# Performance work log

Hardware: AMD Instinct MI355X
Metric: run time of the kernel (lower is better)

The kernel has to match this reference:

```python
import jax, jax.numpy as jnp
import numpy as np

HIDDEN = 100
LAYERS = 10
B, T = 512, 512
INIT = 0.1  # 1/sqrt(hidden_size), torch default uniform bound


def setup_inputs() -> dict:
    key = jax.random.key(0)
    ks = jax.random.split(key, 9)
    u = lambda k, shape: jax.random.uniform(k, shape, jnp.float32, -INIT, INIT)
    return {
        "x": jax.random.normal(ks[0], (B, T, 1), jnp.float32),
        "hidden_state": jnp.zeros((LAYERS, B, HIDDEN), jnp.float32),
        "W_ih0": u(ks[1], (HIDDEN, 1)),
        "W_ih": u(ks[2], (LAYERS - 1, HIDDEN, HIDDEN)),
        "W_hh": u(ks[3], (LAYERS, HIDDEN, HIDDEN)),
        "b_ih": u(ks[4], (LAYERS, HIDDEN)),
        "b_hh": u(ks[5], (LAYERS, HIDDEN)),
        "W_out": u(ks[6], (1, HIDDEN)),
        "b_out": u(ks[7], (1,)),
    }


def reference(x, hidden_state, W_ih0, W_ih, W_hh, b_ih, b_hh, W_out, b_out):
    # Multi-layer tanh RNN (batch_first). Scan over time; fixed loop over 10 layers.
    def step(h, x_t):  # h: [L, B, H], x_t: [B, 1]
        inp = x_t
        new_h = []
        for l in range(LAYERS):
            Wi = W_ih0 if l == 0 else W_ih[l - 1]
            hl = jnp.tanh(inp @ Wi.T + b_ih[l] + h[l] @ W_hh[l].T + b_hh[l])
            new_h.append(hl)
            inp = hl
        return jnp.stack(new_h), inp  # carry, top-layer output [B, H]

    h_final, top = jax.lax.scan(step, hidden_state, jnp.swapaxes(x, 0, 1))
    rnn_output = jnp.swapaxes(top, 0, 1)  # [B, T, H]
    # Per-timestep Linear == one batched matmul
    outs = rnn_output @ W_out.T + b_out  # [B, T, 1]
    return outs, h_final
```

## Files before the change

### kernel.cpp

```cpp
#include <hip/hip_runtime.h>


#define HH   100
#define HS   132
#define HSS  136
#define NL   10
#define NPAIR 5
#define NIF   4
#define BBS  512
#define TTS  512
#define NB   32
#define BC   16
#define NT   512
#define SLOTS (BC * 128)

typedef __attribute__((ext_vector_type(8))) short short8;
typedef __attribute__((ext_vector_type(4))) float f32x4;
typedef __attribute__((ext_vector_type(4))) unsigned int u32x4;

__global__ void init_ws_kernel(int* wsi) {
  int i = blockIdx.x * blockDim.x + threadIdx.x;
  if (i < 16384) wsi[i] = 0;
}

__device__ __forceinline__ int flag_idx(int iface, int chunk) {
  return (iface * NB + chunk) * 16;
}

__device__ __forceinline__ void lds_barrier() {
  __asm__ __volatile__("s_waitcnt lgkmcnt(0)\n\ts_barrier" ::: "memory");
}
__device__ __forceinline__ void ctl_barrier() {
  __asm__ __volatile__("s_barrier" ::: "memory");
}

__device__ __forceinline__ float fast_tanh(float v) {
  float e = __expf(2.0f * v);
  return 1.0f - 2.0f * __builtin_amdgcn_rcpf(e + 1.0f);
}

__device__ __forceinline__ unsigned short bf_rtn(float x) {
  return (unsigned short)((__float_as_uint(x) + 0x8000u) >> 16);
}

__global__ __launch_bounds__(NT, 1) void rnn_pipe(
    const float* __restrict__ x,
    const float* __restrict__ h0,
    const float* __restrict__ Wih0,
    const float* __restrict__ Wih,
    const float* __restrict__ Whh,
    const float* __restrict__ bih,
    const float* __restrict__ bhh,
    const float* __restrict__ Wout,
    const float* __restrict__ bout,
    float* __restrict__ out,
    unsigned short* __restrict__ ring,
    int*   __restrict__ wsi,
    int Kv, int RDv)
{
  const int pair  = blockIdx.x / NB;
  const int chunk = blockIdx.x % NB;
  const int tid   = threadIdx.x;
  const int grp   = tid >> 8;
  const int wtid  = tid & 255;
  const int layer = pair * 2 + grp;
  const int Km = Kv - 1, RDm = RDv - 1;
  const int NE = BC * HH;

  const int wave = wtid >> 6, lane = wtid & 63;
  const int quad = lane >> 4, lp = lane & 15;
  const bool is_l9 = (grp == 1 && pair == NPAIR - 1);

  __shared__ unsigned short hbufL[2][BC][HSS];
  __shared__ unsigned short hbufU[2][BC][HSS];
  __shared__ unsigned short ibufL[2][BC][HSS];
  __shared__ float biasS[2][HS];
  __shared__ float wi0s[HS];
  __shared__ float wouts[HS];
  __shared__ float xin[2][BC];

  for (int i = tid; i < 2 * BC * HSS; i += NT) {
    (&hbufL[0][0][0])[i] = 0; (&hbufU[0][0][0])[i] = 0; (&ibufL[0][0][0])[i] = 0;
  }
  for (int i = wtid; i < HS; i += 256) {
    float bv = 0.f;
    if (i < HH) bv = bih[layer * HH + i] + bhh[layer * HH + i];
    else if (i == 100 && layer == NL - 1) bv = bout[0];
    biasS[grp][i] = bv;
    if (grp == 0) wi0s[i]  = (i < HH) ? Wih0[i] : 0.f;
    else          wouts[i] = (i < HH) ? Wout[i] : 0.f;
  }
  if (tid < BC) { xin[0][tid] = 0.f; xin[1][tid] = 0.f; }
  __syncthreads();
  for (int idx = wtid; idx < NE; idx += 256) {
    unsigned short v =
        bf_rtn(h0[((size_t)layer * BBS + chunk * BC + idx / HH) * HH + idx % HH]);
    if (grp == 0) hbufL[0][idx / HH][idx % HH] = v;
    else          hbufU[1][idx / HH][idx % HH] = v;
  }
  __syncthreads();

  short8 Bf[8][2][2];
  #pragma unroll
  for (int kc = 0; kc < 8; ++kc) {
    #pragma unroll
    for (int ntl = 0; ntl < 2; ++ntl) {
      const int n = wave * 32 + ntl * 16 + lp;
      float wv[8];
      #pragma unroll
      for (int j = 0; j < 8; ++j) {
        const int k = kc * 32 + quad * 8 + j;
        float w = 0.f;
        if (kc < 4) {
          if (k < HH) {
            if (n < HH) w = Whh[(size_t)layer * HH * HH + n * HH + k];
            else if (n == 100 && layer == NL - 1) w = Wout[k];
          }
        } else {
          const int kk = k - 128;
          if (layer > 0 && kk >= 0 && kk < HH && n < HH)
            w = Wih[(size_t)(layer - 1) * HH * HH + n * HH + kk];
        }
        wv[j] = w;
      }
      __attribute__((ext_vector_type(4))) unsigned int p1, p2;
      #pragma unroll
      for (int j2 = 0; j2 < 4; ++j2) {
        unsigned ua = __float_as_uint(wv[2 * j2]), ub = __float_as_uint(wv[2 * j2 + 1]);
        p1[j2] = (ua >> 16) | (ub & 0xFFFF0000u);
        float ra = wv[2 * j2]     - __uint_as_float(ua & 0xFFFF0000u);
        float rb = wv[2 * j2 + 1] - __uint_as_float(ub & 0xFFFF0000u);
        p2[j2] = (__float_as_uint(ra) >> 16) | (__float_as_uint(rb) & 0xFFFF0000u);
      }
      Bf[kc][ntl][0] = __builtin_bit_cast(short8, p1);
      Bf[kc][ntl][1] = __builtin_bit_cast(short8, p2);
    }
  }

  const bool is_cons = (grp == 0 && pair > 0);
  const bool is_prod = (grp == 1 && pair < NPAIR - 1);
  int* prog_in  = is_cons ? wsi + flag_idx(pair - 1, chunk)        : nullptr;
  int* cons_in  = is_cons ? wsi + 8192 + flag_idx(pair - 1, chunk) : nullptr;
  int* prog_out = is_prod ? wsi + flag_idx(pair, chunk)            : nullptr;
  int* cons_out = is_prod ? wsi + 8192 + flag_idx(pair, chunk)     : nullptr;
  unsigned short* ring_in  = is_cons ? ring + (size_t)((pair - 1) * NB + chunk) * RDv * SLOTS : nullptr;
  unsigned short* ring_out = is_prod ? ring + (size_t)(pair * NB + chunk) * RDv * SLOTS       : nullptr;

  const int jcv[2] = { wave * 32 + lp, wave * 32 + 16 + lp };
  const float br[2]  = { biasS[grp][jcv[0]], biasS[grp][jcv[1]] };
  const float w0r[2] = { wi0s[jcv[0]], wi0s[jcv[1]] };
  const float boutv = bout[0];

  f32x4 hreg[2] = {};
  float px = 0.f;
  const int srow = wtid >> 4, scol = (wtid & 15) * 8;

  for (int s = 0; s <= TTS; ++s) {
    const int par = s & 1, nxt = par ^ 1;
    const bool active = (grp == 0) ? (s < TTS) : (s >= 1);
    const int t = (grp == 0) ? s : s - 1;
    const bool bstart = (s < TTS) && ((s & Km) == 0);
    const bool upub   = (s >= 1) && ((s & Km) == 0);

    if (bstart) {
      if (tid == 0 && is_cons) {
        while (__hip_atomic_load(prog_in, __ATOMIC_RELAXED, __HIP_MEMORY_SCOPE_AGENT) < s + Kv)
          __builtin_amdgcn_s_sleep(1);
        (void)__hip_atomic_load(prog_in, __ATOMIC_ACQUIRE, __HIP_MEMORY_SCOPE_AGENT);
      }
      if (tid == 256 && is_prod && s + Kv > RDv) {
        while (__hip_atomic_load(cons_out, __ATOMIC_RELAXED, __HIP_MEMORY_SCOPE_AGENT) < s + Kv - RDv)
          __builtin_amdgcn_s_sleep(1);
      }
      ctl_barrier();
      if (is_cons) {
        u32x4 g = *(const u32x4*)(ring_in + (size_t)(s & RDm) * SLOTS + wtid * 8);
        *(u32x4*)&ibufL[par][srow][scol] = g;
      }
      if (grp == 0 && pair == 0 && s == 0) {
        if (wtid < BC) xin[0][wtid] = x[(size_t)(chunk * BC + wtid) * TTS];
      }
      lds_barrier();
    }

    if (is_prod && s >= 2 && ((s - 1) & Km) != 0) {
      u32x4 v = *(const u32x4*)&hbufU[par][srow][scol];
      *(u32x4*)(ring_out + (size_t)((s - 2) & RDm) * SLOTS + wtid * 8) = v;
    }

    u32x4 pv = {};
    bool pre = false;
    if (is_cons && s < TTS && ((s & Km) != Km) && s + 1 < TTS) {
      pv = *(const u32x4*)(ring_in + (size_t)((s + 1) & RDm) * SLOTS + wtid * 8);
      pre = true;
    }
    if (grp == 0 && pair == 0 && s + 1 < TTS && wtid < BC)
      px = x[(size_t)(chunk * BC + wtid) * TTS + (s + 1)];

    if (active) {
      const unsigned short (*myH)[HSS] = (grp == 0) ? hbufL[par] : hbufU[par];
      const unsigned short (*myI)[HSS] = (grp == 0) ? ibufL[par] : hbufL[par];
      short8 Ah[4], AiS[4];
      #pragma unroll
      for (int kc = 0; kc < 4; ++kc)
        Ah[kc] = *(const short8*)&myH[lp][kc * 32 + quad * 8];
      const bool has_in = (grp == 1) || (pair > 0);
      if (has_in) {
        #pragma unroll
        for (int kc = 0; kc < 4; ++kc)
          AiS[kc] = *(const short8*)&myI[lp][kc * 32 + quad * 8];
      } else {
        #pragma unroll
        for (int kc = 0; kc < 4; ++kc) AiS[kc] = short8{};
      }

      f32x4 a1[2], a2[2] = {}, c1[2] = {}, c2[2] = {};
      #pragma unroll
      for (int ntl = 0; ntl < 2; ++ntl)
        a1[ntl] = (f32x4){br[ntl], br[ntl], br[ntl], br[ntl]};
      if (has_in) {
        #pragma unroll
        for (int kc = 0; kc < 4; ++kc) {
          #pragma unroll
          for (int ntl = 0; ntl < 2; ++ntl) {
            c2[ntl] = __builtin_amdgcn_mfma_f32_16x16x32_bf16(AiS[kc], Bf[kc + 4][ntl][1], c2[ntl], 0, 0, 0);
            c1[ntl] = __builtin_amdgcn_mfma_f32_16x16x32_bf16(AiS[kc], Bf[kc + 4][ntl][0], c1[ntl], 0, 0, 0);
          }
        }
      }
      #pragma unroll
      for (int kc = 0; kc < 4; ++kc) {
        #pragma unroll
        for (int ntl = 0; ntl < 2; ++ntl) {
          a2[ntl] = __builtin_amdgcn_mfma_f32_16x16x32_bf16(Ah[kc], Bf[kc][ntl][1], a2[ntl], 0, 0, 0);
          a1[ntl] = __builtin_amdgcn_mfma_f32_16x16x32_bf16(Ah[kc], Bf[kc][ntl][0], a1[ntl], 0, 0, 0);
        }
      }

      unsigned short (*myHn)[HSS] = (grp == 0) ? hbufL[nxt] : hbufU[nxt];
      #pragma unroll
      for (int ntl = 0; ntl < 2; ++ntl) {
        f32x4 sum = (a1[ntl] + a2[ntl]) + (c1[ntl] + c2[ntl]);
        #pragma unroll
        for (int r = 0; r < 4; ++r) {
          const int m = quad * 4 + r;
          float v = sum[r];
          if (layer == 0) v += xin[par][m] * w0r[ntl];
          if (is_l9 && jcv[ntl] == 100) {
            if (s >= 2)
              out[(size_t)(chunk * BC + m) * TTS + (s - 2)] = v;
          } else {
            float h = fast_tanh(v);
            hreg[ntl][r] = h;
            if (jcv[ntl] < HH) myHn[m][jcv[ntl]] = bf_rtn(h);
          }
        }
      }

      if (t == TTS - 1) {
        #pragma unroll
        for (int ntl = 0; ntl < 2; ++ntl)
          if (jcv[ntl] < HH)
            #pragma unroll
            for (int r = 0; r < 4; ++r)
              out[(size_t)BBS * TTS +
                  ((size_t)layer * BBS + chunk * BC + quad * 4 + r) * HH + jcv[ntl]] =
                  hreg[ntl][r];
      }
    }

    if (pre) *(u32x4*)&ibufL[nxt][srow][scol] = pv;
    if (grp == 0 && pair == 0 && s + 1 < TTS && wtid < BC) xin[nxt][wtid] = px;

    if (upub) {
      lds_barrier();
      if (is_prod) {
        u32x4 v = *(const u32x4*)&hbufU[nxt][srow][scol];
        *(u32x4*)(ring_out + (size_t)((s - 1) & RDm) * SLOTS + wtid * 8) = v;
      }
      __syncthreads();
      if (tid == 256 && is_prod)
        __hip_atomic_store(prog_out, s, __ATOMIC_RELEASE, __HIP_MEMORY_SCOPE_AGENT);
      if (tid == 0 && is_cons)
        __hip_atomic_store(cons_in, s, __ATOMIC_RELAXED, __HIP_MEMORY_SCOPE_AGENT);
    } else {
      lds_barrier();
    }
  }

  if (is_l9) {
    const int b = wtid >> 4, seg = wtid & 15;
    float sacc = 0.f;
    #pragma unroll
    for (int jj = 0; jj < 7; ++jj) {
      const int j = seg * 7 + jj;
      if (j < HH) {
        float h = __uint_as_float((unsigned)hbufU[1][b][j] << 16);
        sacc += h * wouts[j];
      }
    }
    sacc += __shfl_xor(sacc, 1, 16);
    sacc += __shfl_xor(sacc, 2, 16);
    sacc += __shfl_xor(sacc, 4, 16);
    sacc += __shfl_xor(sacc, 8, 16);
    if ((wtid & 15) == 0)
      out[(size_t)(chunk * BC + b) * TTS + (TTS - 1)] = sacc + boutv;
  }
}

extern "C" void kernel_launch(void* const* d_in, const int* in_sizes, int n_in,
                              void* d_out, int out_size, void* d_ws, size_t ws_size,
                              hipStream_t stream) {
  const float* x    = (const float*)d_in[0];
  const float* h0   = (const float*)d_in[1];
  const float* Wih0 = (const float*)d_in[2];
  const float* Wih  = (const float*)d_in[3];
  const float* Whh  = (const float*)d_in[4];
  const float* bih  = (const float*)d_in[5];
  const float* bhh  = (const float*)d_in[6];
  const float* Wout = (const float*)d_in[7];
  const float* bout = (const float*)d_in[8];
  float* out = (float*)d_out;

  int* wsi = (int*)d_ws;
  unsigned short* ring = (unsigned short*)((char*)d_ws + 65536);

  const size_t slot_bytes = (size_t)SLOTS * 2;
  int RDv = 32;
  while (RDv > 2 && 65536 + (size_t)NIF * NB * RDv * slot_bytes > ws_size)
    RDv >>= 1;
  int Kv = RDv / 4;
  if (Kv < 1) Kv = 1;

  hipLaunchKernelGGL(init_ws_kernel, dim3(64), dim3(256), 0, stream, wsi);
  hipLaunchKernelGGL(rnn_pipe, dim3(NPAIR * NB), dim3(NT), 0, stream,
                     x, h0, Wih0, Wih, Whh, bih, bhh, Wout, bout, out, ring, wsi,
                     Kv, RDv);
}
```

Before: 1.056 ms.

## Drop split-bf16 weight residual MFMAs and prefetch ring blocks one step early

Weights were held as a high/low bf16 pair, which doubled the MFMA count on the recurrent critical path. They are now a single round-to-nearest bf16 value, halving the matrix work per step and the weight registers. The block-boundary handshake now waits one step ahead, and the ring read is always prefetched, which removes a barrier and global load from the step's critical path. The cost is reduced weight precision, which may raise error across 512 timesteps and 10 layers.

```diff
diff --git a/kernel.cpp b/kernel.cpp
--- a/kernel.cpp
+++ b/kernel.cpp
@@ -98,9 +98,8 @@
     if (grp == 0) hbufL[0][idx / HH][idx % HH] = v;
     else          hbufU[1][idx / HH][idx % HH] = v;
   }
-  __syncthreads();
-
-  short8 Bf[8][2][2];
+
+  short8 Bf[8][2];
   #pragma unroll
   for (int kc = 0; kc < 8; ++kc) {
     #pragma unroll
@@ -123,17 +122,11 @@
         }
         wv[j] = w;
       }
-      __attribute__((ext_vector_type(4))) unsigned int p1, p2;
-      #pragma unroll
-      for (int j2 = 0; j2 < 4; ++j2) {
-        unsigned ua = __float_as_uint(wv[2 * j2]), ub = __float_as_uint(wv[2 * j2 + 1]);
-        p1[j2] = (ua >> 16) | (ub & 0xFFFF0000u);
-        float ra = wv[2 * j2]     - __uint_as_float(ua & 0xFFFF0000u);
-        float rb = wv[2 * j2 + 1] - __uint_as_float(ub & 0xFFFF0000u);
-        p2[j2] = (__float_as_uint(ra) >> 16) | (__float_as_uint(rb) & 0xFFFF0000u);
-      }
-      Bf[kc][ntl][0] = __builtin_bit_cast(short8, p1);
-      Bf[kc][ntl][1] = __builtin_bit_cast(short8, p2);
+      __attribute__((ext_vector_type(4))) unsigned int p1;
+      #pragma unroll
+      for (int j2 = 0; j2 < 4; ++j2)
+        p1[j2] = (unsigned)bf_rtn(wv[2 * j2]) | ((unsigned)bf_rtn(wv[2 * j2 + 1]) << 16);
+      Bf[kc][ntl] = __builtin_bit_cast(short8, p1);
     }
   }
 
@@ -155,32 +148,38 @@
   float px = 0.f;
   const int srow = wtid >> 4, scol = (wtid & 15) * 8;
 
+  if (tid == 0 && is_cons) {
+    while (__hip_atomic_load(prog_in, __ATOMIC_RELAXED, __HIP_MEMORY_SCOPE_AGENT) < Kv)
+      __builtin_amdgcn_s_sleep(1);
+    (void)__hip_atomic_load(prog_in, __ATOMIC_ACQUIRE, __HIP_MEMORY_SCOPE_AGENT);
+  }
+  ctl_barrier();
+  if (is_cons) {
+    u32x4 g = *(const u32x4*)(ring_in + wtid * 8);
+    *(u32x4*)&ibufL[0][srow][scol] = g;
+  }
+  if (grp == 0 && pair == 0 && wtid < BC)
+    xin[0][wtid] = x[(size_t)(chunk * BC + wtid) * TTS];
+  __syncthreads();
+
   for (int s = 0; s <= TTS; ++s) {
     const int par = s & 1, nxt = par ^ 1;
     const bool active = (grp == 0) ? (s < TTS) : (s >= 1);
     const int t = (grp == 0) ? s : s - 1;
-    const bool bstart = (s < TTS) && ((s & Km) == 0);
-    const bool upub   = (s >= 1) && ((s & Km) == 0);
-
-    if (bstart) {
+    const bool preb = ((s & Km) == Km) && (s + 1 < TTS);
+    const bool upub = (s >= 1) && ((s & Km) == 0);
+
+    if (preb) {
       if (tid == 0 && is_cons) {
-        while (__hip_atomic_load(prog_in, __ATOMIC_RELAXED, __HIP_MEMORY_SCOPE_AGENT) < s + Kv)
+        while (__hip_atomic_load(prog_in, __ATOMIC_RELAXED, __HIP_MEMORY_SCOPE_AGENT) < s + 1 + Kv)
           __builtin_amdgcn_s_sleep(1);
         (void)__hip_atomic_load(prog_in, __ATOMIC_ACQUIRE, __HIP_MEMORY_SCOPE_AGENT);
       }
-      if (tid == 256 && is_prod && s + Kv > RDv) {
-        while (__hip_atomic_load(cons_out, __ATOMIC_RELAXED, __HIP_MEMORY_SCOPE_AGENT) < s + Kv - RDv)
+      if (tid == 256 && is_prod && s + 1 + Kv > RDv) {
+        while (__hip_atomic_load(cons_out, __ATOMIC_RELAXED, __HIP_MEMORY_SCOPE_AGENT) < s + 1 + Kv - RDv)
           __builtin_amdgcn_s_sleep(1);
       }
       ctl_barrier();
-      if (is_cons) {
-        u32x4 g = *(const u32x4*)(ring_in + (size_t)(s & RDm) * SLOTS + wtid * 8);
-        *(u32x4*)&ibufL[par][srow][scol] = g;
-      }
-      if (grp == 0 && pair == 0 && s == 0) {
-        if (wtid < BC) xin[0][wtid] = x[(size_t)(chunk * BC + wtid) * TTS];
-      }
-      lds_barrier();
     }
 
     if (is_prod && s >= 2 && ((s - 1) & Km) != 0) {
@@ -190,7 +189,7 @@
 
     u32x4 pv = {};
     bool pre = false;
-    if (is_cons && s < TTS && ((s & Km) != Km) && s + 1 < TTS) {
+    if (is_cons && s + 1 < TTS) {
       pv = *(const u32x4*)(ring_in + (size_t)((s + 1) & RDm) * SLOTS + wtid * 8);
       pre = true;
     }
@@ -214,7 +213,7 @@
         for (int kc = 0; kc < 4; ++kc) AiS[kc] = short8{};
       }
 
-      f32x4 a1[2], a2[2] = {}, c1[2] = {}, c2[2] = {};
+      f32x4 a1[2], c1[2] = {};
       #pragma unroll
       for (int ntl = 0; ntl < 2; ++ntl)
         a1[ntl] = (f32x4){br[ntl], br[ntl], br[ntl], br[ntl]};
@@ -222,25 +221,21 @@
         #pragma unroll
         for (int kc = 0; kc < 4; ++kc) {
           #pragma unroll
-          for (int ntl = 0; ntl < 2; ++ntl) {
-            c2[ntl] = __builtin_amdgcn_mfma_f32_16x16x32_bf16(AiS[kc], Bf[kc + 4][ntl][1], c2[ntl], 0, 0, 0);
-            c1[ntl] = __builtin_amdgcn_mfma_f32_16x16x32_bf16(AiS[kc], Bf[kc + 4][ntl][0], c1[ntl], 0, 0, 0);
-          }
+          for (int ntl = 0; ntl < 2; ++ntl)
+            c1[ntl] = __builtin_amdgcn_mfma_f32_16x16x32_bf16(AiS[kc], Bf[kc + 4][ntl], c1[ntl], 0, 0, 0);
         }
       }
       #pragma unroll
       for (int kc = 0; kc < 4; ++kc) {
         #pragma unroll
-        for (int ntl = 0; ntl < 2; ++ntl) {
-          a2[ntl] = __builtin_amdgcn_mfma_f32_16x16x32_bf16(Ah[kc], Bf[kc][ntl][1], a2[ntl], 0, 0, 0);
-          a1[ntl] = __builtin_amdgcn_mfma_f32_16x16x32_bf16(Ah[kc], Bf[kc][ntl][0], a1[ntl], 0, 0, 0);
-        }
+        for (int ntl = 0; ntl < 2; ++ntl)
+          a1[ntl] = __builtin_amdgcn_mfma_f32_16x16x32_bf16(Ah[kc], Bf[kc][ntl], a1[ntl], 0, 0, 0);
       }
 
       unsigned short (*myHn)[HSS] = (grp == 0) ? hbufL[nxt] : hbufU[nxt];
       #pragma unroll
       for (int ntl = 0; ntl < 2; ++ntl) {
-        f32x4 sum = (a1[ntl] + a2[ntl]) + (c1[ntl] + c2[ntl]);
+        f32x4 sum = a1[ntl] + c1[ntl];
         #pragma unroll
         for (int r = 0; r < 4; ++r) {
           const int m = quad * 4 + r;
```

Result: faster. 882.5 us, median of 3 (-16.4%).
